# Performance work log

Hardware: AMD Instinct MI355X
Metric: run time of the kernel (lower is better)

The kernel has to match this reference:

```python
import jax, jax.numpy as jnp
import numpy as np

OUT = 7          # output_size
SR = 2           # sampling_ratio
SCALES = (0.25, 0.125, 0.0625, 0.03125)
K_MIN, K_MAX = 2, 5   # -log2(scales[0]), -log2(scales[-1])
CANON_SCALE, CANON_LVL, EPS = 224.0, 4.0, 1e-6


def _roi_align_level(feat, b_idx, boxes, scale):
    """ROIAlign (maskrcnn-benchmark, non-aligned) of all boxes on one level.
    feat: [B,C,H,W], b_idx: [N] int, boxes: [N,4] xyxy in image coords.
    Returns [N,C,OUT,OUT]."""
    N = boxes.shape[0]
    H, W = feat.shape[2], feat.shape[3]
    x1 = boxes[:, 0] * scale
    y1 = boxes[:, 1] * scale
    x2 = boxes[:, 2] * scale
    y2 = boxes[:, 3] * scale
    roi_w = jnp.maximum(x2 - x1, 1.0)
    roi_h = jnp.maximum(y2 - y1, 1.0)
    bin_w = roi_w / OUT
    bin_h = roi_h / OUT
    # sample positions inside each bin, in bin units: [OUT*SR]
    sub = (jnp.arange(SR, dtype=feat.dtype) + 0.5) / SR
    grid1d = (jnp.arange(OUT, dtype=feat.dtype)[:, None] + sub[None, :]).reshape(-1)
    ys = y1[:, None] + bin_h[:, None] * grid1d[None, :]   # [N, OUT*SR]
    xs = x1[:, None] + bin_w[:, None] * grid1d[None, :]   # [N, OUT*SR]
    K = OUT * SR
    Yf = jnp.broadcast_to(ys[:, :, None], (N, K, K)).reshape(N, K * K)
    Xf = jnp.broadcast_to(xs[:, None, :], (N, K, K)).reshape(N, K * K)
    valid = (Yf >= -1.0) & (Yf <= H) & (Xf >= -1.0) & (Xf <= W)
    y = jnp.clip(Yf, 0.0, H - 1)
    x = jnp.clip(Xf, 0.0, W - 1)
    y0 = jnp.floor(y).astype(jnp.int32)
    x0 = jnp.floor(x).astype(jnp.int32)
    y1i = jnp.minimum(y0 + 1, H - 1)
    x1i = jnp.minimum(x0 + 1, W - 1)
    ly = y - y0
    lx = x - x0
    hy = 1.0 - ly
    hx = 1.0 - lx
    b = b_idx[:, None]  # [N,1] broadcasts with [N,K*K]
    def g(yi, xi):
        return feat[b, :, yi, xi]  # [N, K*K, C]
    val = (g(y0, x0) * (hy * hx)[..., None]
           + g(y0, x1i) * (hy * lx)[..., None]
           + g(y1i, x0) * (ly * hx)[..., None]
           + g(y1i, x1i) * (ly * lx)[..., None])
    val = jnp.where(valid[..., None], val, 0.0)
    # [N, OUT, SR, OUT, SR, C] -> average sampling points -> [N, OUT, OUT, C]
    val = val.reshape(N, OUT, SR, OUT, SR, -1).mean(axis=(2, 4))
    return jnp.transpose(val, (0, 3, 1, 2))  # [N, C, OUT, OUT]


def _map_levels(boxes):
    # BoxList.area with TO_REMOVE = 1 (xyxy mode)
    area = (boxes[:, 2] - boxes[:, 0] + 1.0) * (boxes[:, 3] - boxes[:, 1] + 1.0)
    s = jnp.sqrt(area)
    lvl = jnp.floor(CANON_LVL + jnp.log2(s / CANON_SCALE + EPS))
    lvl = jnp.clip(lvl, K_MIN, K_MAX)
    return lvl.astype(jnp.int32) - K_MIN  # 0..3


def setup_inputs() -> dict:
    key = jax.random.key(0)
    ks = jax.random.split(key, 10)
    N = 1024
    H_img, W_img = 800.0, 1216.0
    x1 = jax.random.uniform(ks[0], (N,), minval=0.0, maxval=W_img - 64.0)
    y1 = jax.random.uniform(ks[1], (N,), minval=0.0, maxval=H_img - 64.0)
    w = jax.random.uniform(ks[2], (N,), minval=8.0, maxval=500.0)
    h = jax.random.uniform(ks[3], (N,), minval=8.0, maxval=500.0)
    x2 = jnp.minimum(x1 + w, W_img - 1.0)
    y2 = jnp.minimum(y1 + h, H_img - 1.0)
    boxes = jnp.stack([x1, y1, x2, y2], axis=1).astype(jnp.float32)
    box_batch_idx = jnp.sort(jax.random.randint(ks[4], (N,), 0, 2)).astype(jnp.int32)
    f0 = jax.random.normal(ks[5], (2, 256, 200, 304), dtype=jnp.float32)
    f1 = jax.random.normal(ks[6], (2, 256, 100, 152), dtype=jnp.float32)
    f2 = jax.random.normal(ks[7], (2, 256, 50, 76), dtype=jnp.float32)
    f3 = jax.random.normal(ks[8], (2, 256, 25, 38), dtype=jnp.float32)
    return {"f0": f0, "f1": f1, "f2": f2, "f3": f3,
            "boxes": boxes, "box_batch_idx": box_batch_idx}


def reference(f0, f1, f2, f3, boxes, box_batch_idx):
    feats = (f0, f1, f2, f3)
    levels = _map_levels(boxes)  # [N] in 0..3
    out = None
    for lvl, (feat, scale) in enumerate(zip(feats, SCALES)):
        pooled = _roi_align_level(feat, box_batch_idx, boxes, scale)
        mask = (levels == lvl)[:, None, None, None]
        part = jnp.where(mask, pooled, 0.0)
        out = part if out is None else out + part
    return out  # [N, C, OUT, OUT]
```

## Files before the change

kernel.cpp:

```cpp
#include <hip/hip_runtime.h>
#include <math.h>

#define TILE_F 1792
#define B896   896
#define MAXIP  4
#define MAXI   7

typedef __attribute__((address_space(3))) void lds_void;
typedef const __attribute__((address_space(1))) void g_void;

__device__ __forceinline__ void dma16(const float* g, float* l) {
  __builtin_amdgcn_global_load_lds((g_void*)g, (lds_void*)l, 16, 0, 0);
}
#define WC(N) case N: asm volatile("s_waitcnt vmcnt(" #N ")" ::: "memory"); break;
__device__ __forceinline__ void wait_vmcnt(int k) {
  switch (k) {
    WC(0) WC(1) WC(2) WC(3) WC(4) WC(5) WC(6) WC(7)
    default: asm volatile("s_waitcnt vmcnt(8)" ::: "memory"); break;
  }
}

#define COMPUTE_STORE(TP, CC)                                                  \
  if (lane < 49) {                                                             \
    float acc = 0.0f;                                                          \
    _Pragma("unroll")                                                          \
    for (int sy = 0; sy < 2; ++sy) {                                           \
      _Pragma("unroll")                                                        \
      for (int sx = 0; sx < 2; ++sx) {                                         \
        const float w00 = (TP)[rT[sy] + Cc0[sx]];                              \
        const float w01 = (TP)[rT[sy] + Cc1[sx]];                              \
        const float w10 = (TP)[rB[sy] + Cc0[sx]];                              \
        const float w11 = (TP)[rB[sy] + Cc1[sx]];                              \
        const float bil = HY[sy] * (HX[sx] * w00 + LX[sx] * w01)               \
                        + LY[sy] * (HX[sx] * w10 + LX[sx] * w11);              \
        acc += (VY[sy] * VX[sx]) * bil;                                        \
      }                                                                        \
    }                                                                          \
    outp[(CC) * 49] = acc * 0.25f;                                             \
  }

__global__ __launch_bounds__(128) void pooler_kernel(
    const float* __restrict__ f0, const float* __restrict__ f1,
    const float* __restrict__ f2, const float* __restrict__ f3,
    const float* __restrict__ boxes, const int* __restrict__ bidx,
    float* __restrict__ out, int N)
{
  __shared__ __align__(16) float tile[2][TILE_F];
  const int tid  = threadIdx.x;
  const int wave = tid >> 6, lane = tid & 63;
  const int n    = blockIdx.y;
  if (n >= N) return;

  const float bx1 = boxes[4*n+0], by1 = boxes[4*n+1];
  const float bx2 = boxes[4*n+2], by2 = boxes[4*n+3];
  const float area = (bx2 - bx1 + 1.0f) * (by2 - by1 + 1.0f);
  const float s    = sqrtf(area);
  int lvl = (int)floorf(4.0f + log2f(s / 224.0f + 1e-6f));
  lvl = lvl < 2 ? 2 : (lvl > 5 ? 5 : lvl);
  const int li = lvl - 2;

  int H, W; const float* feat; float scale;
  switch (li) {
    case 0:  feat = f0; H = 200; W = 304; scale = 0.25f;    break;
    case 1:  feat = f1; H = 100; W = 152; scale = 0.125f;   break;
    case 2:  feat = f2; H = 50;  W = 76;  scale = 0.0625f;  break;
    default: feat = f3; H = 25;  W = 38;  scale = 0.03125f; break;
  }
  const int b = bidx[n];
  const float x1s = bx1 * scale, y1s = by1 * scale;
  const float roiw = fmaxf(bx2 * scale - x1s, 1.0f);
  const float roih = fmaxf(by2 * scale - y1s, 1.0f);
  const float binw = roiw / 7.0f, binh = roih / 7.0f;
  const float Hm1f = (float)(H - 1), Wm1f = (float)(W - 1);
  const int   Hm1  = H - 1,          Wm1  = W - 1;

  const float yA = fminf(fmaxf(y1s + binh * 0.25f, 0.0f), Hm1f);
  const float yB = fminf(fmaxf(y1s + binh * 6.75f, 0.0f), Hm1f);
  const float xA = fminf(fmaxf(x1s + binw * 0.25f, 0.0f), Wm1f);
  const float xB = fminf(fmaxf(x1s + binw * 6.75f, 0.0f), Wm1f);
  const int y_lo  = (int)yA;
  const int y_hi  = min((int)yB + 1, Hm1);
  const int regH  = y_hi - y_lo + 1;
  const int x_lo4 = ((int)xA) & ~3;
  const int x_hi  = min((int)xB + 1, Wm1);
  const int row4  = ((x_hi - x_lo4 + 4) >> 2);
  const int regW4 = row4 << 2;

  const int bin = (lane < 49) ? lane : 0;
  const int ph = bin / 7, pw = bin - (bin / 7) * 7;
  int   rT[2], rB[2], Cc0[2], Cc1[2];
  int   y0a[2], y1a[2], x0a[2], x1a[2];
  float HY[2], LY[2], VY[2], HX[2], LX[2], VX[2];
#pragma unroll
  for (int t = 0; t < 2; ++t) {
    {
      const float g  = (float)ph + 0.25f + 0.5f * (float)t;
      const float Yf = y1s + binh * g;
      VY[t] = (Yf >= -1.0f && Yf <= (float)H) ? 1.0f : 0.0f;
      const float y = fminf(fmaxf(Yf, 0.0f), Hm1f);
      const int  y0 = (int)y;
      LY[t] = y - (float)y0;  HY[t] = 1.0f - LY[t];
      y0a[t] = y0;  y1a[t] = min(y0 + 1, Hm1);
      rT[t] = (y0 - y_lo) * regW4;
      rB[t] = (y1a[t] - y_lo) * regW4;
    }
    {
      const float g  = (float)pw + 0.25f + 0.5f * (float)t;
      const float Xf = x1s + binw * g;
      VX[t] = (Xf >= -1.0f && Xf <= (float)W) ? 1.0f : 0.0f;
      const float x = fminf(fmaxf(Xf, 0.0f), Wm1f);
      const int  x0 = (int)x;
      LX[t] = x - (float)x0;  HX[t] = 1.0f - LX[t];
      x0a[t] = x0;  x1a[t] = min(x0 + 1, Wm1);
      Cc0[t] = x0 - x_lo4;
      Cc1[t] = x1a[t] - x_lo4;
    }
  }

  const size_t planeHW = (size_t)H * W;
  const int    cbase   = (blockIdx.x << 5) + (wave << 4);
  const float* plane0  = feat + ((size_t)(b * 256 + cbase)) * planeHW
                              + (size_t)y_lo * W;
  float*       outp    = out + ((size_t)n * 256 + cbase) * 49 + lane;
  float*       myt     = tile[wave];

  if (li == 3) {
    int   off[2][2][4];
    float wt [2][2][4];
#pragma unroll
    for (int sy = 0; sy < 2; ++sy) {
#pragma unroll
      for (int sx = 0; sx < 2; ++sx) {
        const float vv = VY[sy] * VX[sx];
        off[sy][sx][0] = y0a[sy] * 38 + x0a[sx];  wt[sy][sx][0] = vv * HY[sy] * HX[sx];
        off[sy][sx][1] = y0a[sy] * 38 + x1a[sx];  wt[sy][sx][1] = vv * HY[sy] * LX[sx];
        off[sy][sx][2] = y1a[sy] * 38 + x0a[sx];  wt[sy][sx][2] = vv * LY[sy] * HX[sx];
        off[sy][sx][3] = y1a[sy] * 38 + x1a[sx];  wt[sy][sx][3] = vv * LY[sy] * LX[sx];
      }
    }
    const float* pc0 = feat + ((size_t)(b * 256 + cbase)) * planeHW;
#pragma unroll 2
    for (int cc = 0; cc < 16; ++cc) {
      const float* pc = pc0 + (size_t)cc * planeHW;
      float acc = 0.0f;
#pragma unroll
      for (int sy = 0; sy < 2; ++sy)
#pragma unroll
        for (int sx = 0; sx < 2; ++sx)
#pragma unroll
          for (int k = 0; k < 4; ++k)
            acc += wt[sy][sx][k] * pc[off[sy][sx][k]];
      if (lane < 49) outp[cc * 49] = acc * 0.25f;
    }
  } else {
    int cnt4 = regH * row4;
    if (cnt4 > TILE_F / 4) cnt4 = TILE_F / 4;
    const int Mrow = (int)(65536.0f / (float)row4) + 1;
    const int K = (cnt4 + 63) >> 6;

    if (cnt4 <= B896 / 4) {
      int soff[MAXIP];
#pragma unroll
      for (int i = 0; i < MAXIP; ++i) {
        const int u = lane + (i << 6);
        if (u < cnt4) {
          const int r = (u * Mrow) >> 16;
          const int c = u - r * row4;
          soff[i] = r * W + x_lo4 + (c << 2);
        } else soff[i] = -1;
      }
#pragma unroll
      for (int i = 0; i < MAXIP; ++i)
        if (soff[i] >= 0) dma16(plane0 + soff[i], myt + (i << 8));

      for (int cc = 0; cc < 16; ++cc) {
        asm volatile("s_waitcnt lgkmcnt(0)" ::: "memory");
        if (cc + 1 < 16) {
          const float* pl = plane0 + (size_t)(cc + 1) * planeHW;
          float* bf = myt + (((cc + 1) & 1) ? B896 : 0);
#pragma unroll
          for (int i = 0; i < MAXIP; ++i)
            if (soff[i] >= 0) dma16(pl + soff[i], bf + (i << 8));
        }
        wait_vmcnt(cc == 0 ? K : (cc == 15 ? 1 : K + 1));
        const float* bufC = myt + ((cc & 1) ? B896 : 0);
        COMPUTE_STORE(bufC, cc)
      }
    } else {
      int soff[MAXI];
#pragma unroll
      for (int i = 0; i < MAXI; ++i) {
        const int u = lane + (i << 6);
        if (u < cnt4) {
          const int r = (u * Mrow) >> 16;
          const int c = u - r * row4;
          soff[i] = r * W + x_lo4 + (c << 2);
        } else soff[i] = -1;
      }
      for (int cc = 0; cc < 16; ++cc) {
        const float* plane = plane0 + (size_t)cc * planeHW;
        asm volatile("s_waitcnt lgkmcnt(0)" ::: "memory");
#pragma unroll
        for (int i = 0; i < MAXI; ++i)
          if (soff[i] >= 0) dma16(plane + soff[i], myt + (i << 8));
        asm volatile("s_waitcnt vmcnt(0)" ::: "memory");
        COMPUTE_STORE(myt, cc)
      }
    }
  }
}

extern "C" void kernel_launch(void* const* d_in, const int* in_sizes, int n_in,
                              void* d_out, int out_size, void* d_ws, size_t ws_size,
                              hipStream_t stream) {
  const float* f0    = (const float*)d_in[0];
  const float* f1    = (const float*)d_in[1];
  const float* f2    = (const float*)d_in[2];
  const float* f3    = (const float*)d_in[3];
  const float* boxes = (const float*)d_in[4];
  const int*   bidx  = (const int*)d_in[5];
  const int N = in_sizes[5];
  dim3 grid(8, N);
  pooler_kernel<<<grid, 128, 0, stream>>>(f0, f1, f2, f3, boxes, bidx,
                                          (float*)d_out, N);
}
```

Measured before the change: 283.7 us.

## Replace LDS-staged region DMA with direct global gathers for all levels

Removes the LDS tile path, which used async global_load_lds copies of the ROI bounding region with double buffering, and the level-specific branches. Every level now gathers its 16 bilinear taps per bin straight from global memory, processing two channels per iteration so more loads are in flight. This drops the LDS footprint and the waitcnt synchronisation, and no longer fetches unused region pixels for large boxes. In exchange it issues scattered, uncoalesced 4-byte gathers that depend on the cache for reuse.

```diff
diff --git a/kernel.cpp b/kernel.cpp
--- a/kernel.cpp
+++ b/kernel.cpp
@@ -1,43 +1,7 @@
 #include <hip/hip_runtime.h>
 #include <math.h>
 
-#define TILE_F 1792
-#define B896   896
-#define MAXIP  4
-#define MAXI   7
 
-typedef __attribute__((address_space(3))) void lds_void;
-typedef const __attribute__((address_space(1))) void g_void;
-
-__device__ __forceinline__ void dma16(const float* g, float* l) {
-  __builtin_amdgcn_global_load_lds((g_void*)g, (lds_void*)l, 16, 0, 0);
-}
-#define WC(N) case N: asm volatile("s_waitcnt vmcnt(" #N ")" ::: "memory"); break;
-__device__ __forceinline__ void wait_vmcnt(int k) {
-  switch (k) {
-    WC(0) WC(1) WC(2) WC(3) WC(4) WC(5) WC(6) WC(7)
-    default: asm volatile("s_waitcnt vmcnt(8)" ::: "memory"); break;
-  }
-}
-
-#define COMPUTE_STORE(TP, CC)                                                  \
-  if (lane < 49) {                                                             \
-    float acc = 0.0f;                                                          \
-    _Pragma("unroll")                                                          \
-    for (int sy = 0; sy < 2; ++sy) {                                           \
-      _Pragma("unroll")                                                        \
-      for (int sx = 0; sx < 2; ++sx) {                                         \
-        const float w00 = (TP)[rT[sy] + Cc0[sx]];                              \
-        const float w01 = (TP)[rT[sy] + Cc1[sx]];                              \
-        const float w10 = (TP)[rB[sy] + Cc0[sx]];                              \
-        const float w11 = (TP)[rB[sy] + Cc1[sx]];                              \
-        const float bil = HY[sy] * (HX[sx] * w00 + LX[sx] * w01)               \
-                        + LY[sy] * (HX[sx] * w10 + LX[sx] * w11);              \
-        acc += (VY[sy] * VX[sx]) * bil;                                        \
-      }                                                                        \
-    }                                                                          \
-    outp[(CC) * 49] = acc * 0.25f;                                             \
-  }
 
 __global__ __launch_bounds__(128) void pooler_kernel(
     const float* __restrict__ f0, const float* __restrict__ f1,
@@ -45,7 +9,6 @@
     const float* __restrict__ boxes, const int* __restrict__ bidx,
     float* __restrict__ out, int N)
 {
-  __shared__ __align__(16) float tile[2][TILE_F];
   const int tid  = threadIdx.x;
   const int wave = tid >> 6, lane = tid & 63;
   const int n    = blockIdx.y;
@@ -74,21 +37,8 @@
   const float Hm1f = (float)(H - 1), Wm1f = (float)(W - 1);
   const int   Hm1  = H - 1,          Wm1  = W - 1;
 
-  const float yA = fminf(fmaxf(y1s + binh * 0.25f, 0.0f), Hm1f);
-  const float yB = fminf(fmaxf(y1s + binh * 6.75f, 0.0f), Hm1f);
-  const float xA = fminf(fmaxf(x1s + binw * 0.25f, 0.0f), Wm1f);
-  const float xB = fminf(fmaxf(x1s + binw * 6.75f, 0.0f), Wm1f);
-  const int y_lo  = (int)yA;
-  const int y_hi  = min((int)yB + 1, Hm1);
-  const int regH  = y_hi - y_lo + 1;
-  const int x_lo4 = ((int)xA) & ~3;
-  const int x_hi  = min((int)xB + 1, Wm1);
-  const int row4  = ((x_hi - x_lo4 + 4) >> 2);
-  const int regW4 = row4 << 2;
-
   const int bin = (lane < 49) ? lane : 0;
   const int ph = bin / 7, pw = bin - (bin / 7) * 7;
-  int   rT[2], rB[2], Cc0[2], Cc1[2];
   int   y0a[2], y1a[2], x0a[2], x1a[2];
   float HY[2], LY[2], VY[2], HX[2], LX[2], VX[2];
 #pragma unroll
@@ -101,8 +51,6 @@
       const int  y0 = (int)y;
       LY[t] = y - (float)y0;  HY[t] = 1.0f - LY[t];
       y0a[t] = y0;  y1a[t] = min(y0 + 1, Hm1);
-      rT[t] = (y0 - y_lo) * regW4;
-      rB[t] = (y1a[t] - y_lo) * regW4;
     }
     {
       const float g  = (float)pw + 0.25f + 0.5f * (float)t;
@@ -112,100 +60,47 @@
       const int  x0 = (int)x;
       LX[t] = x - (float)x0;  HX[t] = 1.0f - LX[t];
       x0a[t] = x0;  x1a[t] = min(x0 + 1, Wm1);
-      Cc0[t] = x0 - x_lo4;
-      Cc1[t] = x1a[t] - x_lo4;
+    }
+  }
+
+  int   off[16];
+  float wt [16];
+#pragma unroll
+  for (int sy = 0; sy < 2; ++sy) {
+#pragma unroll
+    for (int sx = 0; sx < 2; ++sx) {
+      const float vv = VY[sy] * VX[sx];
+      const int q = (sy * 2 + sx) * 4;
+      off[q+0] = y0a[sy] * W + x0a[sx];  wt[q+0] = vv * HY[sy] * HX[sx];
+      off[q+1] = y0a[sy] * W + x1a[sx];  wt[q+1] = vv * HY[sy] * LX[sx];
+      off[q+2] = y1a[sy] * W + x0a[sx];  wt[q+2] = vv * LY[sy] * HX[sx];
+      off[q+3] = y1a[sy] * W + x1a[sx];  wt[q+3] = vv * LY[sy] * LX[sx];
     }
   }
 
   const size_t planeHW = (size_t)H * W;
   const int    cbase   = (blockIdx.x << 5) + (wave << 4);
-  const float* plane0  = feat + ((size_t)(b * 256 + cbase)) * planeHW
-                              + (size_t)y_lo * W;
+  const float* pc0     = feat + ((size_t)(b * 256 + cbase)) * planeHW;
   float*       outp    = out + ((size_t)n * 256 + cbase) * 49 + lane;
-  float*       myt     = tile[wave];
 
-  if (li == 3) {
-    int   off[2][2][4];
-    float wt [2][2][4];
+#pragma unroll 2
+  for (int cp = 0; cp < 8; ++cp) {
+    const int ccA = cp * 2, ccB = ccA + 1;
+    const float* pA = pc0 + (size_t)ccA * planeHW;
+    const float* pB = pc0 + (size_t)ccB * planeHW;
+    float vA[16], vB[16];
 #pragma unroll
-    for (int sy = 0; sy < 2; ++sy) {
+    for (int k = 0; k < 16; ++k) vA[k] = pA[off[k]];
 #pragma unroll
-      for (int sx = 0; sx < 2; ++sx) {
-        const float vv = VY[sy] * VX[sx];
-        off[sy][sx][0] = y0a[sy] * 38 + x0a[sx];  wt[sy][sx][0] = vv * HY[sy] * HX[sx];
-        off[sy][sx][1] = y0a[sy] * 38 + x1a[sx];  wt[sy][sx][1] = vv * HY[sy] * LX[sx];
-        off[sy][sx][2] = y1a[sy] * 38 + x0a[sx];  wt[sy][sx][2] = vv * LY[sy] * HX[sx];
-        off[sy][sx][3] = y1a[sy] * 38 + x1a[sx];  wt[sy][sx][3] = vv * LY[sy] * LX[sx];
-      }
-    }
-    const float* pc0 = feat + ((size_t)(b * 256 + cbase)) * planeHW;
-#pragma unroll 2
-    for (int cc = 0; cc < 16; ++cc) {
-      const float* pc = pc0 + (size_t)cc * planeHW;
-      float acc = 0.0f;
+    for (int k = 0; k < 16; ++k) vB[k] = pB[off[k]];
+    float aA = 0.0f, aB = 0.0f;
 #pragma unroll
-      for (int sy = 0; sy < 2; ++sy)
+    for (int k = 0; k < 16; ++k) aA += wt[k] * vA[k];
 #pragma unroll
-        for (int sx = 0; sx < 2; ++sx)
-#pragma unroll
-          for (int k = 0; k < 4; ++k)
-            acc += wt[sy][sx][k] * pc[off[sy][sx][k]];
-      if (lane < 49) outp[cc * 49] = acc * 0.25f;
-    }
-  } else {
-    int cnt4 = regH * row4;
-    if (cnt4 > TILE_F / 4) cnt4 = TILE_F / 4;
-    const int Mrow = (int)(65536.0f / (float)row4) + 1;
-    const int K = (cnt4 + 63) >> 6;
-
-    if (cnt4 <= B896 / 4) {
-      int soff[MAXIP];
-#pragma unroll
-      for (int i = 0; i < MAXIP; ++i) {
-        const int u = lane + (i << 6);
-        if (u < cnt4) {
-          const int r = (u * Mrow) >> 16;
-          const int c = u - r * row4;
-          soff[i] = r * W + x_lo4 + (c << 2);
-        } else soff[i] = -1;
-      }
-#pragma unroll
-      for (int i = 0; i < MAXIP; ++i)
-        if (soff[i] >= 0) dma16(plane0 + soff[i], myt + (i << 8));
-
-      for (int cc = 0; cc < 16; ++cc) {
-        asm volatile("s_waitcnt lgkmcnt(0)" ::: "memory");
-        if (cc + 1 < 16) {
-          const float* pl = plane0 + (size_t)(cc + 1) * planeHW;
-          float* bf = myt + (((cc + 1) & 1) ? B896 : 0);
-#pragma unroll
-          for (int i = 0; i < MAXIP; ++i)
-            if (soff[i] >= 0) dma16(pl + soff[i], bf + (i << 8));
-        }
-        wait_vmcnt(cc == 0 ? K : (cc == 15 ? 1 : K + 1));
-        const float* bufC = myt + ((cc & 1) ? B896 : 0);
-        COMPUTE_STORE(bufC, cc)
-      }
-    } else {
-      int soff[MAXI];
-#pragma unroll
-      for (int i = 0; i < MAXI; ++i) {
-        const int u = lane + (i << 6);
-        if (u < cnt4) {
-          const int r = (u * Mrow) >> 16;
-          const int c = u - r * row4;
-          soff[i] = r * W + x_lo4 + (c << 2);
-        } else soff[i] = -1;
-      }
-      for (int cc = 0; cc < 16; ++cc) {
-        const float* plane = plane0 + (size_t)cc * planeHW;
-        asm volatile("s_waitcnt lgkmcnt(0)" ::: "memory");
-#pragma unroll
-        for (int i = 0; i < MAXI; ++i)
-          if (soff[i] >= 0) dma16(plane + soff[i], myt + (i << 8));
-        asm volatile("s_waitcnt vmcnt(0)" ::: "memory");
-        COMPUTE_STORE(myt, cc)
-      }
+    for (int k = 0; k < 16; ++k) aB += wt[k] * vB[k];
+    if (lane < 49) {
+      outp[ccA * 49] = aA * 0.25f;
+      outp[ccB * 49] = aB * 0.25f;
     }
   }
 }
```

Result: slower. 348.4 us (+22.8%).

## Prefetch all feature maps into cache via dummy LDS DMA loads

Applied to the files above, without the earlier changes.

Each wave issues global_load_lds DMA reads over a strided slice of every FPN feature map into a per-wave dummy LDS buffer. Together the grid sweeps the full feature tensors through the cache hierarchy before the ROI gathers. The intent is to turn scattered gather misses into cache hits. The cost is streaming all feature data once and extra outstanding loads, which are reflected in a widened vmcnt wait table.

```diff
diff --git a/kernel.cpp b/kernel.cpp
--- a/kernel.cpp
+++ b/kernel.cpp
@@ -6,6 +6,16 @@
 #define MAXIP  4
 #define MAXI   7
 
+#define NF4_0 7782400
+#define NF4_1 1945600
+#define NF4_2 486400
+#define NF4_3 121600
+#define PFW   16384
+#define SH_0  475
+#define SH_1  119
+#define SH_2  30
+#define SH_3  8
+
 typedef __attribute__((address_space(3))) void lds_void;
 typedef const __attribute__((address_space(1))) void g_void;
 
@@ -15,8 +25,8 @@
 #define WC(N) case N: asm volatile("s_waitcnt vmcnt(" #N ")" ::: "memory"); break;
 __device__ __forceinline__ void wait_vmcnt(int k) {
   switch (k) {
-    WC(0) WC(1) WC(2) WC(3) WC(4) WC(5) WC(6) WC(7)
-    default: asm volatile("s_waitcnt vmcnt(8)" ::: "memory"); break;
+    WC(0) WC(1) WC(2) WC(3) WC(4) WC(5) WC(6) WC(7) WC(8) WC(9) WC(10) WC(11)
+    default: asm volatile("s_waitcnt vmcnt(12)" ::: "memory"); break;
   }
 }
 
@@ -46,6 +56,7 @@
     float* __restrict__ out, int N)
 {
   __shared__ __align__(16) float tile[2][TILE_F];
+  __shared__ __align__(16) float dummy[2][256];
   const int tid  = threadIdx.x;
   const int wave = tid >> 6, lane = tid & 63;
   const int n    = blockIdx.y;
@@ -53,6 +64,27 @@
 
   const float bx1 = boxes[4*n+0], by1 = boxes[4*n+1];
   const float bx2 = boxes[4*n+2], by2 = boxes[4*n+3];
+  const int b = bidx[n];
+
+  {
+    float* dmy = dummy[wave];
+    const int wid = (blockIdx.y * gridDim.x + blockIdx.x) * 2 + wave;
+#define PF(F, NF4, SH, ITERS)                                                  \
+    { const int start = wid * (SH);                                            \
+      _Pragma("unroll")                                                        \
+      for (int i = 0; i < (ITERS); ++i) {                                      \
+        const int u = (i << 6) + lane;                                         \
+        const int idx = start + u;                                             \
+        if (u < (SH) && idx < (NF4))                                           \
+          dma16((F) + ((size_t)idx << 2), dmy);                                \
+      } }
+    PF(f0, NF4_0, SH_0, 8)
+    PF(f1, NF4_1, SH_1, 2)
+    PF(f2, NF4_2, SH_2, 1)
+    PF(f3, NF4_3, SH_3, 1)
+#undef PF
+  }
+
   const float area = (bx2 - bx1 + 1.0f) * (by2 - by1 + 1.0f);
   const float s    = sqrtf(area);
   int lvl = (int)floorf(4.0f + log2f(s / 224.0f + 1e-6f));
@@ -66,7 +98,6 @@
     case 2:  feat = f2; H = 50;  W = 76;  scale = 0.0625f;  break;
     default: feat = f3; H = 25;  W = 38;  scale = 0.03125f; break;
   }
-  const int b = bidx[n];
   const float x1s = bx1 * scale, y1s = by1 * scale;
   const float roiw = fmaxf(bx2 * scale - x1s, 1.0f);
   const float roih = fmaxf(by2 * scale - y1s, 1.0f);
```

New measurement: 290.5 us. +2.4%, slower.
